# Performance work log

Measured on AMD Instinct MI355X. Metric: run time of the kernel, lower is better.

## Reference

```python
import jax, jax.numpy as jnp
import numpy as np

B, T, C = 2, 2048, 2048
N_HEAD, KV_HEADS = 16, 4
HEAD_DIM = C // N_HEAD  # 128
EPS = 1e-6


def setup_inputs() -> dict:
    key = jax.random.key(0)
    ks = jax.random.split(key, 3)
    x = jax.random.normal(ks[0], (B, T, C), dtype=jnp.float32)
    qkv_out = (N_HEAD + 2 * KV_HEADS) * HEAD_DIM  # 3072
    w_qkv = jax.random.normal(ks[1], (qkv_out, C), dtype=jnp.float32) * 0.02
    w_proj = jax.random.normal(ks[2], (C, C), dtype=jnp.float32) * 0.02
    q_norm_w = jnp.ones((HEAD_DIM,), dtype=jnp.float32)
    k_norm_w = jnp.ones((HEAD_DIM,), dtype=jnp.float32)
    # RoPE frequencies: theta = 10000^{-2i/d}, angles = pos * theta
    inv_freq = 1.0 / (10000.0 ** (np.arange(0, HEAD_DIM, 2, dtype=np.float32) / HEAD_DIM))
    angles = np.arange(T, dtype=np.float32)[:, None] * inv_freq[None, :]  # [T, 64]
    freqs_cos = jnp.asarray(np.cos(angles), dtype=jnp.float32)
    freqs_sin = jnp.asarray(np.sin(angles), dtype=jnp.float32)
    return {"x": x, "w_qkv": w_qkv, "w_proj": w_proj,
            "q_norm_w": q_norm_w, "k_norm_w": k_norm_w,
            "freqs_cos": freqs_cos, "freqs_sin": freqs_sin}


def _rope(t, cos, sin):
    # t: [B, H, T, D]; interpret last dim as D/2 complex pairs (a, b)
    a = t[..., 0::2]
    b = t[..., 1::2]
    oa = a * cos - b * sin
    ob = a * sin + b * cos
    return jnp.stack([oa, ob], axis=-1).reshape(t.shape)


def _rmsnorm(t, w, eps=EPS):
    rms = jnp.sqrt(jnp.mean(t * t, axis=-1, keepdims=True) + eps)
    return w * (t / rms)


def reference(x, w_qkv, w_proj, q_norm_w, k_norm_w, freqs_cos, freqs_sin):
    b, t, c = x.shape
    hd = HEAD_DIM
    qkv = x @ w_qkv.T  # [B, T, 3072]
    q_size = N_HEAD * hd
    kv_size = KV_HEADS * hd
    q = qkv[..., :q_size].reshape(b, t, N_HEAD, hd).transpose(0, 2, 1, 3)
    k = qkv[..., q_size:q_size + kv_size].reshape(b, t, KV_HEADS, hd).transpose(0, 2, 1, 3)
    v = qkv[..., q_size + kv_size:].reshape(b, t, KV_HEADS, hd).transpose(0, 2, 1, 3)
    # repeat_interleave KV heads to match query heads (GQA)
    rep = N_HEAD // KV_HEADS
    k = jnp.repeat(k, rep, axis=1)
    v = jnp.repeat(v, rep, axis=1)
    # RoPE (applied after repeat, matching the torch code order)
    cos = freqs_cos[:t][None, None, :, :]
    sin = freqs_sin[:t][None, None, :, :]
    q = _rope(q, cos, sin)
    k = _rope(k, cos, sin)
    # QK RMSNorm per head_dim
    q = _rmsnorm(q, q_norm_w)
    k = _rmsnorm(k, k_norm_w)
    # causal SDPA
    scores = jnp.einsum('bhqd,bhkd->bhqk', q, k) / jnp.sqrt(jnp.float32(hd))
    causal = jnp.tril(jnp.ones((t, t), dtype=bool))
    scores = jnp.where(causal[None, None], scores, jnp.finfo(scores.dtype).min)
    att = jax.nn.softmax(scores, axis=-1)
    y = jnp.einsum('bhqk,bhkd->bhqd', att, v)
    y = y.transpose(0, 2, 1, 3).reshape(b, t, c)
    return y @ w_proj.T
```

## Files before the change

### kernel.cpp

```cpp
#include <hip/hip_runtime.h>
#include <hip/hip_bf16.h>

#define B_    2
#define T_    2048
#define C_    2048
#define NH_   16
#define KVH_  4
#define HD_   128
#define QKV_  3072
#define M_    4096

typedef float  floatx4 __attribute__((ext_vector_type(4)));
typedef __bf16 bf16x8  __attribute__((ext_vector_type(8)));
typedef __bf16 bf16x4  __attribute__((ext_vector_type(4)));
typedef __bf16 bf16x2  __attribute__((ext_vector_type(2)));

typedef const __attribute__((address_space(1))) void* gas_t;
typedef __attribute__((address_space(3))) void*       las_t;
__device__ __forceinline__ void gl_lds16(const void* g, void* l) {
  __builtin_amdgcn_global_load_lds((gas_t)g, (las_t)l, 16, 0, 0);
}

__global__ __launch_bounds__(256) void cvt3(const float* __restrict__ s0, __bf16* __restrict__ d0, int n0,
                                            const float* __restrict__ s1, __bf16* __restrict__ d1, int n1,
                                            const float* __restrict__ s2, __bf16* __restrict__ d2, int n2) {
  int i = blockIdx.x * blockDim.x + threadIdx.x;
  const float* s; __bf16* d;
  if (i < n0) { s = s0; d = d0; }
  else {
    i -= n0;
    if (i < n1) { s = s1; d = d1; }
    else { i -= n1; if (i >= n2) return; s = s2; d = d2; }
  }
  float4 f = ((const float4*)s)[i];
  bf16x4 o = { (__bf16)f.x, (__bf16)f.y, (__bf16)f.z, (__bf16)f.w };
  ((bf16x4*)d)[i] = o;
}

template <typename OutT>
__global__ __launch_bounds__(256) void gemm_bt(const __bf16* __restrict__ A,
                                               const __bf16* __restrict__ Bm,
                                               OutT* __restrict__ Cc,
                                               int N, int K) {
  __shared__ __align__(16) __bf16 As[2][128 * 32];
  __shared__ __align__(16) __bf16 Bs[2][128 * 32];
  const int tid  = threadIdx.x;
  const int wid  = tid >> 6, lane = tid & 63, quad = lane >> 4, r16 = lane & 15;
  const int bm   = blockIdx.y * 128, bn = blockIdx.x * 128;
  const int wm   = (wid >> 1) * 64, wn = (wid & 1) * 64;
  const int srow = wid * 16 + (lane >> 2);
  const int scol = (lane & 3) * 8;
  const __bf16* aptr = A  + (size_t)(bm + srow) * K + scol;
  const __bf16* bptr = Bm + (size_t)(bn + srow) * K + scol;
  const size_t rowskip = (size_t)64 * K;

  floatx4 acc[4][4];
  #pragma unroll
  for (int i = 0; i < 4; i++)
    #pragma unroll
    for (int j = 0; j < 4; j++) acc[i][j] = (floatx4){0.f, 0.f, 0.f, 0.f};

  for (int k0 = 0; k0 < K; k0 += 64) {
    #pragma unroll
    for (int hf = 0; hf < 2; hf++) {
      gl_lds16(aptr + k0 + hf * 32,           &As[hf][wid * 512]);
      gl_lds16(aptr + rowskip + k0 + hf * 32, &As[hf][2048 + wid * 512]);
      gl_lds16(bptr + k0 + hf * 32,           &Bs[hf][wid * 512]);
      gl_lds16(bptr + rowskip + k0 + hf * 32, &Bs[hf][2048 + wid * 512]);
    }
    __syncthreads();

    #pragma unroll
    for (int hf = 0; hf < 2; hf++) {
      bf16x8 af[4], bfr[4];
      #pragma unroll
      for (int i = 0; i < 4; i++) af[i]  = *(const bf16x8*)&As[hf][(wm + i * 16 + r16) * 32 + quad * 8];
      #pragma unroll
      for (int j = 0; j < 4; j++) bfr[j] = *(const bf16x8*)&Bs[hf][(wn + j * 16 + r16) * 32 + quad * 8];
      #pragma unroll
      for (int i = 0; i < 4; i++)
        #pragma unroll
        for (int j = 0; j < 4; j++)
          acc[i][j] = __builtin_amdgcn_mfma_f32_16x16x32_bf16(af[i], bfr[j], acc[i][j], 0, 0, 0);
    }
    __syncthreads();
  }

  #pragma unroll
  for (int i = 0; i < 4; i++) {
    #pragma unroll
    for (int reg = 0; reg < 4; reg++) {
      int row = bm + wm + i * 16 + quad * 4 + reg;
      OutT* crow = Cc + (size_t)row * N + bn + wn;
      #pragma unroll
      for (int j = 0; j < 4; j++) crow[j * 16 + r16] = (OutT)acc[i][j][reg];
    }
  }
}

__global__ __launch_bounds__(256) void rope_norm(const __bf16* __restrict__ qkv,
                                                 const float* __restrict__ qw,
                                                 const float* __restrict__ kw,
                                                 const float* __restrict__ fc,
                                                 const float* __restrict__ fs,
                                                 __bf16* __restrict__ qn,
                                                 __bf16* __restrict__ kn) {
  const int tid  = threadIdx.x;
  const int wid  = tid >> 6, lane = tid & 63;
  const int row  = blockIdx.x * 4 + wid;
  const int b    = row >> 11, t = row & (T_ - 1);
  const float cs = fc[t * 64 + lane], sn = fs[t * 64 + lane];
  const __bf16* base = qkv + (size_t)row * QKV_;

  #pragma unroll 2
  for (int h = 0; h < NH_; h++) {
    bf16x2 ab = *(const bf16x2*)(base + h * HD_ + 2 * lane);
    float ax = (float)ab[0], ay = (float)ab[1];
    float oa = ax * cs - ay * sn;
    float ob = ax * sn + ay * cs;
    float ss = oa * oa + ob * ob;
    #pragma unroll
    for (int off = 32; off; off >>= 1) ss += __shfl_xor(ss, off);
    float rinv = rsqrtf(ss * (1.0f / HD_) + 1e-6f);
    bf16x2 o = { (__bf16)(oa * rinv * qw[2 * lane]), (__bf16)(ob * rinv * qw[2 * lane + 1]) };
    *(bf16x2*)&qn[(size_t)((b * NH_ + h) * T_ + t) * HD_ + 2 * lane] = o;
  }
  #pragma unroll 2
  for (int h = 0; h < KVH_; h++) {
    bf16x2 ab = *(const bf16x2*)(base + C_ + h * HD_ + 2 * lane);
    float ax = (float)ab[0], ay = (float)ab[1];
    float oa = ax * cs - ay * sn;
    float ob = ax * sn + ay * cs;
    float ss = oa * oa + ob * ob;
    #pragma unroll
    for (int off = 32; off; off >>= 1) ss += __shfl_xor(ss, off);
    float rinv = rsqrtf(ss * (1.0f / HD_) + 1e-6f);
    bf16x2 o = { (__bf16)(oa * rinv * kw[2 * lane]), (__bf16)(ob * rinv * kw[2 * lane + 1]) };
    *(bf16x2*)&kn[(size_t)((b * KVH_ + h) * T_ + t) * HD_ + 2 * lane] = o;
  }
}

__global__ __launch_bounds__(256) void vtrans(const __bf16* __restrict__ qkv,
                                              __bf16* __restrict__ vT) {
  __shared__ __bf16 L[64 * 68];
  const int tid = threadIdx.x;
  const int t0 = blockIdx.x * 64;
  const int d0 = blockIdx.y * 64;
  const int z  = blockIdx.z;
  const int b  = z >> 2, hk = z & 3;
  const int srcc = C_ + KVH_ * HD_ + hk * HD_ + d0;
  const int rr = tid >> 4, c4 = (tid & 15) * 4;
  #pragma unroll
  for (int i = 0; i < 4; i++) {
    int t = rr + i * 16;
    bf16x4 f = *(const bf16x4*)&qkv[(size_t)(b * T_ + t0 + t) * QKV_ + srcc + c4];
    *(bf16x4*)&L[t * 68 + c4] = f;
  }
  __syncthreads();
  const int dr = tid >> 3, tc8 = (tid & 7) * 8;
  #pragma unroll
  for (int i = 0; i < 2; i++) {
    int d = dr + i * 32;
    bf16x8 ov;
    #pragma unroll
    for (int j = 0; j < 8; j++) ov[j] = L[(tc8 + j) * 68 + d];
    *(bf16x8*)&vT[(size_t)(z * HD_ + d0 + d) * T_ + t0 + tc8] = ov;
  }
}

__device__ __forceinline__ int swz_w(int lane) {
  return ((lane & 3) << 4) | ((lane >> 2) ^ ((lane & 3) << 1));
}
__device__ __forceinline__ int swz_r(int quad, int r16) {
  return (quad << 4) | (r16 ^ (quad << 1));
}

__device__ __forceinline__ void kv_prefetch8(const __bf16* kbase, const __bf16* vbase,
                                             int kt0, int wid, int lane,
                                             bf16x8 kreg[2], bf16x8 vreg[2]) {
  const int r4 = lane >> 2, c8 = (lane & 3) * 8;
  #pragma unroll
  for (int i = 0; i < 2; i++) {
    const int n = wid * 2 + i;
    kreg[i] = *(const bf16x8*)&kbase[(size_t)(kt0 + (n >> 2) * 16 + r4) * HD_ + (n & 3) * 32 + c8];
    vreg[i] = *(const bf16x8*)&vbase[(size_t)((n >> 1) * 16 + r4) * T_ + kt0 + (n & 1) * 32 + c8];
  }
}

__device__ __forceinline__ void kv_commit8(__bf16* Ks, __bf16* Vs, int wid, int lane,
                                           const bf16x8 kreg[2], const bf16x8 vreg[2]) {
  const int slot = swz_w(lane);
  #pragma unroll
  for (int i = 0; i < 2; i++) {
    *(bf16x8*)(Ks + (wid * 2 + i) * 512 + slot * 8) = kreg[i];
    *(bf16x8*)(Vs + (wid * 2 + i) * 512 + slot * 8) = vreg[i];
  }
}

__global__ __launch_bounds__(512, 4) void flash(const __bf16* __restrict__ q,
                                                const __bf16* __restrict__ k,
                                                const __bf16* __restrict__ vT,
                                                __bf16* __restrict__ y) {
  __shared__ __align__(16) __bf16 Ks[2][64 * 128];
  __shared__ __align__(16) __bf16 Vs[2][64 * 128];
  __shared__ __align__(16) __bf16 Ps[8][16 * 48];
  const int tid = threadIdx.x;
  const int wid = tid >> 6, lane = tid & 63, quad = lane >> 4, r16 = lane & 15;
  const int x   = blockIdx.x;
  const int p   = (x >> 5) & 7, hl = x & 31;
  const int qt  = (x < 256) ? (15 - p) : p;
  const int b = hl >> 4, h = hl & 15, hk = h >> 2;

  const __bf16* kbase = k  + (size_t)(b * KVH_ + hk) * T_ * HD_;
  const __bf16* vbase = vT + (size_t)(b * KVH_ + hk) * HD_ * T_;
  __bf16* Pw = Ps[wid];
  const float sc = 0.08838834764831845f;
  const float NEG = -__builtin_inff();
  bf16x8 ones;
  #pragma unroll
  for (int i = 0; i < 8; i++) ones[i] = (__bf16)1.0f;

  const int nt = 2 * (qt + 1);
  const int r0 = qt * 128 + wid * 16;

  const __bf16* qrow = q + ((size_t)(b * NH_ + h) * T_ + r0 + r16) * HD_;
  bf16x8 qf[4];
  #pragma unroll
  for (int kb = 0; kb < 4; kb++) qf[kb] = *(const bf16x8*)&qrow[kb * 32 + quad * 8];

  floatx4 o[8], ol = (floatx4){0.f, 0.f, 0.f, 0.f};
  #pragma unroll
  for (int j = 0; j < 8; j++) o[j] = (floatx4){0.f, 0.f, 0.f, 0.f};
  float m_r[4] = {NEG, NEG, NEG, NEG};

  bf16x8 kreg[2], vreg[2];
  kv_prefetch8(kbase, vbase, 0, wid, lane, kreg, vreg);
  kv_commit8(&Ks[0][0], &Vs[0][0], wid, lane, kreg, vreg);
  if (nt > 1) kv_prefetch8(kbase, vbase, 64, wid, lane, kreg, vreg);
  __syncthreads();

  #pragma unroll 1
  for (int it = 0; it < nt; ++it) {
    if (it + 1 < nt) {
      kv_commit8(&Ks[(it + 1) & 1][0], &Vs[(it + 1) & 1][0], wid, lane, kreg, vreg);
      if (it + 2 < nt) kv_prefetch8(kbase, vbase, (it + 2) * 64, wid, lane, kreg, vreg);
    }

    const int kt0 = it * 64;
    const __bf16* Kb = &Ks[it & 1][0];
    const __bf16* Vb = &Vs[it & 1][0];
    if (kt0 <= r0 + 15) {
      floatx4 s[4];
      #pragma unroll
      for (int cb = 0; cb < 4; cb++) s[cb] = (floatx4){0.f, 0.f, 0.f, 0.f};
      __builtin_amdgcn_s_setprio(1);
      #pragma unroll
      for (int kb = 0; kb < 4; kb++)
        #pragma unroll
        for (int cb = 0; cb < 4; cb++) {
          bf16x8 kf = *(const bf16x8*)&Kb[(cb * 4 + kb) * 512 + swz_r(quad, r16) * 8];
          s[cb] = __builtin_amdgcn_mfma_f32_16x16x32_bf16(qf[kb], kf, s[cb], 0, 0, 0);
        }
      __builtin_amdgcn_s_setprio(0);

      const bool needmask = (kt0 + 63 > r0);
      #pragma unroll
      for (int reg = 0; reg < 4; reg++) {
        const int rowq = r0 + quad * 4 + reg;
        s[0][reg] *= sc; s[1][reg] *= sc; s[2][reg] *= sc; s[3][reg] *= sc;
        if (needmask) {
          if (kt0 +      r16 > rowq) s[0][reg] = NEG;
          if (kt0 + 16 + r16 > rowq) s[1][reg] = NEG;
          if (kt0 + 32 + r16 > rowq) s[2][reg] = NEG;
          if (kt0 + 48 + r16 > rowq) s[3][reg] = NEG;
        }
      }
      float mx[4], mnew[4];
      #pragma unroll
      for (int reg = 0; reg < 4; reg++) {
        float m0 = fmaxf(fmaxf(s[0][reg], s[1][reg]), fmaxf(s[2][reg], s[3][reg]));
        #pragma unroll
        for (int off = 8; off; off >>= 1) m0 = fmaxf(m0, __shfl_xor(m0, off));
        mx[reg] = m0;
        mnew[reg] = fmaxf(m_r[reg], m0);
      }
      float growth = fmaxf(fmaxf(mx[0] - m_r[0], mx[1] - m_r[1]),
                           fmaxf(mx[2] - m_r[2], mx[3] - m_r[3]));
      if (!__all(growth <= 8.0f)) {
        #pragma unroll
        for (int reg = 0; reg < 4; reg++) {
          float a = __expf(m_r[reg] - mnew[reg]);
          m_r[reg] = mnew[reg];
          ol[reg] *= a;
          #pragma unroll
          for (int j = 0; j < 8; j++) o[j][reg] *= a;
        }
      }
      #pragma unroll
      for (int c = 0; c < 2; c++) {
        #pragma unroll
        for (int reg = 0; reg < 4; reg++) {
          const int prow = quad * 4 + reg;
          Pw[prow * 48 +      r16] = (__bf16)__expf(s[2 * c    ][reg] - m_r[reg]);
          Pw[prow * 48 + 16 + r16] = (__bf16)__expf(s[2 * c + 1][reg] - m_r[reg]);
        }
        __asm__ volatile("" ::: "memory");
        bf16x8 pf = *(const bf16x8*)&Pw[r16 * 48 + quad * 8];
        __builtin_amdgcn_s_setprio(1);
        ol = __builtin_amdgcn_mfma_f32_16x16x32_bf16(pf, ones, ol, 0, 0, 0);
        #pragma unroll
        for (int j = 0; j < 8; j++) {
          bf16x8 vf = *(const bf16x8*)&Vb[(j * 2 + c) * 512 + swz_r(quad, r16) * 8];
          o[j] = __builtin_amdgcn_mfma_f32_16x16x32_bf16(pf, vf, o[j], 0, 0, 0);
        }
        __builtin_amdgcn_s_setprio(0);
        __asm__ volatile("" ::: "memory");
      }
    }
    __syncthreads();
  }

  #pragma unroll
  for (int reg = 0; reg < 4; reg++) {
    int trow = r0 + quad * 4 + reg;
    float inv = 1.0f / ol[reg];
    __bf16* yr = y + ((size_t)(b * T_) + trow) * C_ + h * HD_;
    #pragma unroll
    for (int j = 0; j < 8; j++) yr[j * 16 + r16] = (__bf16)(o[j][reg] * inv);
  }
}

extern "C" void kernel_launch(void* const* d_in, const int* in_sizes, int n_in,
                              void* d_out, int out_size, void* d_ws, size_t ws_size,
                              hipStream_t stream) {
  const float* x     = (const float*)d_in[0];
  const float* wqkv  = (const float*)d_in[1];
  const float* wproj = (const float*)d_in[2];
  const float* qw    = (const float*)d_in[3];
  const float* kw    = (const float*)d_in[4];
  const float* fc    = (const float*)d_in[5];
  const float* fs    = (const float*)d_in[6];
  float* out = (float*)d_out;

  char* w = (char*)d_ws;
  __bf16* xb     = (__bf16*)w; w += (size_t)M_ * C_ * 2;
  __bf16* wqkvb  = (__bf16*)w; w += (size_t)QKV_ * C_ * 2;
  __bf16* wprojb = (__bf16*)w; w += (size_t)C_ * C_ * 2;
  __bf16* qkv    = (__bf16*)w; w += (size_t)M_ * QKV_ * 2;
  __bf16* qn     = (__bf16*)w; w += (size_t)B_ * NH_ * T_ * HD_ * 2;
  __bf16* kn     = (__bf16*)w; w += (size_t)B_ * KVH_ * T_ * HD_ * 2;
  __bf16* vT     = (__bf16*)w; w += (size_t)B_ * KVH_ * T_ * HD_ * 2;
  __bf16* ybf    = (__bf16*)w; w += (size_t)M_ * C_ * 2;

  const int n0 = M_ * C_ / 4, n1 = QKV_ * C_ / 4, n2 = C_ * C_ / 4;
  cvt3<<<(n0 + n1 + n2 + 255) / 256, 256, 0, stream>>>(x, xb, n0, wqkv, wqkvb, n1, wproj, wprojb, n2);

  gemm_bt<__bf16><<<dim3(QKV_ / 128, M_ / 128), 256, 0, stream>>>(xb, wqkvb, qkv, QKV_, C_);
  rope_norm<<<M_ / 4, 256, 0, stream>>>(qkv, qw, kw, fc, fs, qn, kn);
  vtrans<<<dim3(T_ / 64, HD_ / 64, B_ * KVH_), 256, 0, stream>>>(qkv, vT);
  flash<<<dim3(512), 512, 0, stream>>>(qn, kn, vT, ybf);
  gemm_bt<float><<<dim3(C_ / 128, M_ / 128), 256, 0, stream>>>(ybf, wprojb, out, C_, C_);
}
```

Measured before the change: 322.5 us.

## Add 256x256 tiled GEMM with 10-slot LDS ring pipeline for QKV projection

Adds a new 512-thread GEMM kernel that uses 256x256 output tiles and a 10-slot LDS ring buffer. Half-tiles are staged with direct global-to-LDS loads, interleaved with four MFMA phases per K step, and s_setprio raises priority around the MFMA work. The kernel replaces the 128x128 GEMM for the QKV projection only. Larger tiles improve data reuse, but the grid shrinks to 12x16=192 blocks, fewer than the CU count, so the GPU may be underutilized, and the large shared-memory ring limits occupancy.

```diff
diff --git a/kernel.cpp b/kernel.cpp
--- a/kernel.cpp
+++ b/kernel.cpp
@@ -98,6 +98,165 @@
   }
 }
 
+template <typename OutT>
+__global__ __launch_bounds__(512, 2) void gemm256(const __bf16* __restrict__ A,
+                                                  const __bf16* __restrict__ Bm,
+                                                  OutT* __restrict__ Cc,
+                                                  int N, int K) {
+  __shared__ __align__(16) __bf16 ring[10 * 8192];
+  const int tid  = threadIdx.x;
+  const int lane = tid & 63, quad = lane >> 4, r16 = lane & 15;
+  const int wid  = tid >> 6;
+  const int wm   = wid >> 2, wn = wid & 3;
+  const int bm   = blockIdx.y * 256, bn = blockIdx.x * 256;
+  const int nt   = K >> 6;
+  const int wbase = tid & ~63;
+  const int lb   = (wn & 1) * 4;
+
+  floatx4 acc[8][4];
+  #pragma unroll
+  for (int i = 0; i < 8; i++)
+    #pragma unroll
+    for (int j = 0; j < 4; j++) acc[i][j] = (floatx4){0.f, 0.f, 0.f, 0.f};
+
+  auto stage = [&](int h, int slot) {
+    const int kt = h >> 2, q = h & 3;
+    const __bf16* gb = (q < 2) ? (A  + (size_t)(bm + (q << 7)) * K)
+                               : (Bm + (size_t)(bn + ((q - 2) << 7)) * K);
+    #pragma unroll
+    for (int is = 0; is < 2; is++) {
+      const int s   = is * 512 + tid;
+      const int lrh = s >> 7, cc = (s >> 4) & 7, sl = s & 15;
+      const int lr  = lrh * 16 + (sl ^ cc);
+      gl_lds16(gb + (size_t)lr * K + (kt << 6) + (cc << 3),
+               &ring[slot * 8192 + (is * 512 + wbase) * 8]);
+    }
+  };
+
+  #pragma unroll 1
+  for (int h = 0; h < 6; ++h)
+    if (h < 4 * nt) stage(h, h);
+
+  #pragma unroll 1
+  for (int j = 0; j < nt; ++j) {
+    if (j + 1 < nt) { asm volatile("s_waitcnt vmcnt(4)" ::: "memory"); }
+    else            { asm volatile("s_waitcnt vmcnt(0)" ::: "memory"); }
+    __builtin_amdgcn_s_barrier();
+    asm volatile("" ::: "memory");
+
+    const int b4 = (4 * j) % 10;
+    const __bf16* Ah = &ring[((b4 + wm) % 10) * 8192];
+    const __bf16* Bh = &ring[((b4 + 2 + (wn >> 1)) % 10) * 8192];
+    const int h0 = 4 * j + 6, hend = 4 * nt;
+
+    bf16x8 af[4][2], bfr[2][2];
+
+    #pragma unroll
+    for (int i = 0; i < 4; i++)
+      #pragma unroll
+      for (int ks = 0; ks < 2; ks++) {
+        const int cc = ks * 4 + quad;
+        af[i][ks] = *(const bf16x8*)&Ah[i * 1024 + cc * 128 + ((r16 ^ cc) << 3)];
+      }
+    #pragma unroll
+    for (int i = 0; i < 2; i++)
+      #pragma unroll
+      for (int ks = 0; ks < 2; ks++) {
+        const int cc = ks * 4 + quad;
+        bfr[i][ks] = *(const bf16x8*)&Bh[(lb + i) * 1024 + cc * 128 + ((r16 ^ cc) << 3)];
+      }
+    if (h0 < hend) stage(h0, (b4 + 6) % 10);
+    __builtin_amdgcn_s_barrier();
+    __builtin_amdgcn_s_setprio(1);
+    #pragma unroll
+    for (int ks = 0; ks < 2; ks++)
+      #pragma unroll
+      for (int i = 0; i < 4; i++)
+        #pragma unroll
+        for (int jj = 0; jj < 2; jj++)
+          acc[i][jj] = __builtin_amdgcn_mfma_f32_16x16x32_bf16(af[i][ks], bfr[jj][ks], acc[i][jj], 0, 0, 0);
+    __builtin_amdgcn_s_setprio(0);
+    __builtin_amdgcn_s_barrier();
+
+    #pragma unroll
+    for (int i = 0; i < 2; i++)
+      #pragma unroll
+      for (int ks = 0; ks < 2; ks++) {
+        const int cc = ks * 4 + quad;
+        bfr[i][ks] = *(const bf16x8*)&Bh[(lb + 2 + i) * 1024 + cc * 128 + ((r16 ^ cc) << 3)];
+      }
+    if (h0 + 1 < hend) stage(h0 + 1, (b4 + 7) % 10);
+    __builtin_amdgcn_s_barrier();
+    __builtin_amdgcn_s_setprio(1);
+    #pragma unroll
+    for (int ks = 0; ks < 2; ks++)
+      #pragma unroll
+      for (int i = 0; i < 4; i++)
+        #pragma unroll
+        for (int jj = 0; jj < 2; jj++)
+          acc[i][2 + jj] = __builtin_amdgcn_mfma_f32_16x16x32_bf16(af[i][ks], bfr[jj][ks], acc[i][2 + jj], 0, 0, 0);
+    __builtin_amdgcn_s_setprio(0);
+    __builtin_amdgcn_s_barrier();
+
+    #pragma unroll
+    for (int i = 0; i < 4; i++)
+      #pragma unroll
+      for (int ks = 0; ks < 2; ks++) {
+        const int cc = ks * 4 + quad;
+        af[i][ks] = *(const bf16x8*)&Ah[(4 + i) * 1024 + cc * 128 + ((r16 ^ cc) << 3)];
+      }
+    #pragma unroll
+    for (int i = 0; i < 2; i++)
+      #pragma unroll
+      for (int ks = 0; ks < 2; ks++) {
+        const int cc = ks * 4 + quad;
+        bfr[i][ks] = *(const bf16x8*)&Bh[(lb + i) * 1024 + cc * 128 + ((r16 ^ cc) << 3)];
+      }
+    if (h0 + 2 < hend) stage(h0 + 2, (b4 + 8) % 10);
+    __builtin_amdgcn_s_barrier();
+    __builtin_amdgcn_s_setprio(1);
+    #pragma unroll
+    for (int ks = 0; ks < 2; ks++)
+      #pragma unroll
+      for (int i = 0; i < 4; i++)
+        #pragma unroll
+        for (int jj = 0; jj < 2; jj++)
+          acc[4 + i][jj] = __builtin_amdgcn_mfma_f32_16x16x32_bf16(af[i][ks], bfr[jj][ks], acc[4 + i][jj], 0, 0, 0);
+    __builtin_amdgcn_s_setprio(0);
+    __builtin_amdgcn_s_barrier();
+
+    #pragma unroll
+    for (int i = 0; i < 2; i++)
+      #pragma unroll
+      for (int ks = 0; ks < 2; ks++) {
+        const int cc = ks * 4 + quad;
+        bfr[i][ks] = *(const bf16x8*)&Bh[(lb + 2 + i) * 1024 + cc * 128 + ((r16 ^ cc) << 3)];
+      }
+    if (h0 + 3 < hend) stage(h0 + 3, (b4 + 9) % 10);
+    __builtin_amdgcn_s_barrier();
+    __builtin_amdgcn_s_setprio(1);
+    #pragma unroll
+    for (int ks = 0; ks < 2; ks++)
+      #pragma unroll
+      for (int i = 0; i < 4; i++)
+        #pragma unroll
+        for (int jj = 0; jj < 2; jj++)
+          acc[4 + i][2 + jj] = __builtin_amdgcn_mfma_f32_16x16x32_bf16(af[i][ks], bfr[jj][ks], acc[4 + i][2 + jj], 0, 0, 0);
+    __builtin_amdgcn_s_setprio(0);
+    __builtin_amdgcn_s_barrier();
+  }
+
+  #pragma unroll
+  for (int mi = 0; mi < 8; mi++)
+    #pragma unroll
+    for (int reg = 0; reg < 4; reg++) {
+      const int row = bm + wm * 128 + mi * 16 + quad * 4 + reg;
+      OutT* crow = Cc + (size_t)row * N + bn + wn * 64;
+      #pragma unroll
+      for (int ni = 0; ni < 4; ni++) crow[ni * 16 + r16] = (OutT)acc[mi][ni][reg];
+    }
+}
+
 __global__ __launch_bounds__(256) void rope_norm(const __bf16* __restrict__ qkv,
                                                  const float* __restrict__ qw,
                                                  const float* __restrict__ kw,
@@ -355,7 +514,7 @@
   const int n0 = M_ * C_ / 4, n1 = QKV_ * C_ / 4, n2 = C_ * C_ / 4;
   cvt3<<<(n0 + n1 + n2 + 255) / 256, 256, 0, stream>>>(x, xb, n0, wqkv, wqkvb, n1, wproj, wprojb, n2);
 
-  gemm_bt<__bf16><<<dim3(QKV_ / 128, M_ / 128), 256, 0, stream>>>(xb, wqkvb, qkv, QKV_, C_);
+  gemm256<__bf16><<<dim3(QKV_ / 256, M_ / 256), 512, 0, stream>>>(xb, wqkvb, qkv, QKV_, C_);
   rope_norm<<<M_ / 4, 256, 0, stream>>>(qkv, qw, kw, fc, fs, qn, kn);
   vtrans<<<dim3(T_ / 64, HD_ / 64, B_ * KVH_), 256, 0, stream>>>(qkv, vT);
   flash<<<dim3(512), 512, 0, stream>>>(qn, kn, vT, ybf);
```

Measured after the change: 322.1 us. About the same (-0.1%).

## Double-buffer GEMM LDS with swizzle and vmcnt pipelining; merge rope and V-transpose

Applied to the files above, without the earlier changes.

Rewrites the bf16 GEMM so the next K-tile's global-to-LDS loads are issued before computing on the current tile. It uses two LDS stages of 128x64, an XOR-swizzled layout to avoid bank conflicts, s_waitcnt vmcnt for partial waits, and setprio around the MFMA blocks. It also fuses the rope/RMSNorm and V-transpose kernels into one launch with a block-index split, removing one launch. LDS use doubles to 64KB per block, which may limit occupancy despite launch_bounds(256,2).

```diff
diff --git a/kernel.cpp b/kernel.cpp
--- a/kernel.cpp
+++ b/kernel.cpp
@@ -38,21 +38,21 @@
 }
 
 template <typename OutT>
-__global__ __launch_bounds__(256) void gemm_bt(const __bf16* __restrict__ A,
-                                               const __bf16* __restrict__ Bm,
-                                               OutT* __restrict__ Cc,
-                                               int N, int K) {
-  __shared__ __align__(16) __bf16 As[2][128 * 32];
-  __shared__ __align__(16) __bf16 Bs[2][128 * 32];
+__global__ __launch_bounds__(256, 2) void gemm_cnt(const __bf16* __restrict__ A,
+                                                   const __bf16* __restrict__ Bm,
+                                                   OutT* __restrict__ Cc,
+                                                   int N, int K) {
+  __shared__ __align__(16) __bf16 As[2][128 * 64];
+  __shared__ __align__(16) __bf16 Bs[2][128 * 64];
   const int tid  = threadIdx.x;
   const int wid  = tid >> 6, lane = tid & 63, quad = lane >> 4, r16 = lane & 15;
   const int bm   = blockIdx.y * 128, bn = blockIdx.x * 128;
   const int wm   = (wid >> 1) * 64, wn = (wid & 1) * 64;
-  const int srow = wid * 16 + (lane >> 2);
-  const int scol = (lane & 3) * 8;
-  const __bf16* aptr = A  + (size_t)(bm + srow) * K + scol;
-  const __bf16* bptr = Bm + (size_t)(bn + srow) * K + scol;
-  const size_t rowskip = (size_t)64 * K;
+  const int srow = tid >> 3;
+  const int clog = (tid & 7) ^ (srow & 7);
+  const __bf16* aR = A  + (size_t)(bm + srow) * K + clog * 8;
+  const __bf16* bR = Bm + (size_t)(bn + srow) * K + clog * 8;
+  const int nt = K >> 6;
 
   floatx4 acc[4][4];
   #pragma unroll
@@ -60,30 +60,48 @@
     #pragma unroll
     for (int j = 0; j < 4; j++) acc[i][j] = (floatx4){0.f, 0.f, 0.f, 0.f};
 
-  for (int k0 = 0; k0 < K; k0 += 64) {
+  auto stage = [&](int s, int k0) {
+    #pragma unroll
+    for (int p = 0; p < 4; p++) {
+      gl_lds16(aR + (size_t)(p * 32) * K + k0, &As[s][(p * 32 + wid * 8) * 64]);
+      gl_lds16(bR + (size_t)(p * 32) * K + k0, &Bs[s][(p * 32 + wid * 8) * 64]);
+    }
+  };
+
+  stage(0, 0);
+
+  #pragma unroll 1
+  for (int j = 0; j < nt; ++j) {
+    if (j + 1 < nt) {
+      stage((j + 1) & 1, (j + 1) << 6);
+      asm volatile("s_waitcnt vmcnt(8)" ::: "memory");
+    } else {
+      asm volatile("s_waitcnt vmcnt(0)" ::: "memory");
+    }
+    __builtin_amdgcn_s_barrier();
+    asm volatile("" ::: "memory");
+
+    const __bf16* Ab = As[j & 1];
+    const __bf16* Bb = Bs[j & 1];
     #pragma unroll
     for (int hf = 0; hf < 2; hf++) {
-      gl_lds16(aptr + k0 + hf * 32,           &As[hf][wid * 512]);
-      gl_lds16(aptr + rowskip + k0 + hf * 32, &As[hf][2048 + wid * 512]);
-      gl_lds16(bptr + k0 + hf * 32,           &Bs[hf][wid * 512]);
-      gl_lds16(bptr + rowskip + k0 + hf * 32, &Bs[hf][2048 + wid * 512]);
-    }
-    __syncthreads();
-
-    #pragma unroll
-    for (int hf = 0; hf < 2; hf++) {
+      const int xo = (((hf << 2) + quad) ^ (r16 & 7)) << 3;
       bf16x8 af[4], bfr[4];
       #pragma unroll
-      for (int i = 0; i < 4; i++) af[i]  = *(const bf16x8*)&As[hf][(wm + i * 16 + r16) * 32 + quad * 8];
-      #pragma unroll
-      for (int j = 0; j < 4; j++) bfr[j] = *(const bf16x8*)&Bs[hf][(wn + j * 16 + r16) * 32 + quad * 8];
+      for (int i = 0; i < 4; i++) af[i]  = *(const bf16x8*)&Ab[(wm + i * 16 + r16) * 64 + xo];
+      #pragma unroll
+      for (int i = 0; i < 4; i++) bfr[i] = *(const bf16x8*)&Bb[(wn + i * 16 + r16) * 64 + xo];
+      __builtin_amdgcn_s_setprio(1);
       #pragma unroll
       for (int i = 0; i < 4; i++)
         #pragma unroll
-        for (int j = 0; j < 4; j++)
-          acc[i][j] = __builtin_amdgcn_mfma_f32_16x16x32_bf16(af[i], bfr[j], acc[i][j], 0, 0, 0);
-    }
-    __syncthreads();
+        for (int jj = 0; jj < 4; jj++)
+          acc[i][jj] = __builtin_amdgcn_mfma_f32_16x16x32_bf16(af[i], bfr[jj], acc[i][jj], 0, 0, 0);
+      __builtin_amdgcn_s_setprio(0);
+    }
+    asm volatile("" ::: "memory");
+    __builtin_amdgcn_s_barrier();
+    asm volatile("" ::: "memory");
   }
 
   #pragma unroll
@@ -98,55 +116,55 @@
   }
 }
 
-__global__ __launch_bounds__(256) void rope_norm(const __bf16* __restrict__ qkv,
-                                                 const float* __restrict__ qw,
-                                                 const float* __restrict__ kw,
-                                                 const float* __restrict__ fc,
-                                                 const float* __restrict__ fs,
-                                                 __bf16* __restrict__ qn,
-                                                 __bf16* __restrict__ kn) {
-  const int tid  = threadIdx.x;
-  const int wid  = tid >> 6, lane = tid & 63;
-  const int row  = blockIdx.x * 4 + wid;
-  const int b    = row >> 11, t = row & (T_ - 1);
-  const float cs = fc[t * 64 + lane], sn = fs[t * 64 + lane];
-  const __bf16* base = qkv + (size_t)row * QKV_;
-
-  #pragma unroll 2
-  for (int h = 0; h < NH_; h++) {
-    bf16x2 ab = *(const bf16x2*)(base + h * HD_ + 2 * lane);
-    float ax = (float)ab[0], ay = (float)ab[1];
-    float oa = ax * cs - ay * sn;
-    float ob = ax * sn + ay * cs;
-    float ss = oa * oa + ob * ob;
-    #pragma unroll
-    for (int off = 32; off; off >>= 1) ss += __shfl_xor(ss, off);
-    float rinv = rsqrtf(ss * (1.0f / HD_) + 1e-6f);
-    bf16x2 o = { (__bf16)(oa * rinv * qw[2 * lane]), (__bf16)(ob * rinv * qw[2 * lane + 1]) };
-    *(bf16x2*)&qn[(size_t)((b * NH_ + h) * T_ + t) * HD_ + 2 * lane] = o;
-  }
-  #pragma unroll 2
-  for (int h = 0; h < KVH_; h++) {
-    bf16x2 ab = *(const bf16x2*)(base + C_ + h * HD_ + 2 * lane);
-    float ax = (float)ab[0], ay = (float)ab[1];
-    float oa = ax * cs - ay * sn;
-    float ob = ax * sn + ay * cs;
-    float ss = oa * oa + ob * ob;
-    #pragma unroll
-    for (int off = 32; off; off >>= 1) ss += __shfl_xor(ss, off);
-    float rinv = rsqrtf(ss * (1.0f / HD_) + 1e-6f);
-    bf16x2 o = { (__bf16)(oa * rinv * kw[2 * lane]), (__bf16)(ob * rinv * kw[2 * lane + 1]) };
-    *(bf16x2*)&kn[(size_t)((b * KVH_ + h) * T_ + t) * HD_ + 2 * lane] = o;
-  }
-}
-
-__global__ __launch_bounds__(256) void vtrans(const __bf16* __restrict__ qkv,
+__global__ __launch_bounds__(256) void ropevt(const __bf16* __restrict__ qkv,
+                                              const float* __restrict__ qw,
+                                              const float* __restrict__ kw,
+                                              const float* __restrict__ fc,
+                                              const float* __restrict__ fs,
+                                              __bf16* __restrict__ qn,
+                                              __bf16* __restrict__ kn,
                                               __bf16* __restrict__ vT) {
   __shared__ __bf16 L[64 * 68];
   const int tid = threadIdx.x;
-  const int t0 = blockIdx.x * 64;
-  const int d0 = blockIdx.y * 64;
-  const int z  = blockIdx.z;
+  if (blockIdx.x < M_ / 4) {
+    const int wid  = tid >> 6, lane = tid & 63;
+    const int row  = blockIdx.x * 4 + wid;
+    const int b    = row >> 11, t = row & (T_ - 1);
+    const float cs = fc[t * 64 + lane], sn = fs[t * 64 + lane];
+    const __bf16* base = qkv + (size_t)row * QKV_;
+
+    #pragma unroll 2
+    for (int h = 0; h < NH_; h++) {
+      bf16x2 ab = *(const bf16x2*)(base + h * HD_ + 2 * lane);
+      float ax = (float)ab[0], ay = (float)ab[1];
+      float oa = ax * cs - ay * sn;
+      float ob = ax * sn + ay * cs;
+      float ss = oa * oa + ob * ob;
+      #pragma unroll
+      for (int off = 32; off; off >>= 1) ss += __shfl_xor(ss, off);
+      float rinv = rsqrtf(ss * (1.0f / HD_) + 1e-6f);
+      bf16x2 o = { (__bf16)(oa * rinv * qw[2 * lane]), (__bf16)(ob * rinv * qw[2 * lane + 1]) };
+      *(bf16x2*)&qn[(size_t)((b * NH_ + h) * T_ + t) * HD_ + 2 * lane] = o;
+    }
+    #pragma unroll 2
+    for (int h = 0; h < KVH_; h++) {
+      bf16x2 ab = *(const bf16x2*)(base + C_ + h * HD_ + 2 * lane);
+      float ax = (float)ab[0], ay = (float)ab[1];
+      float oa = ax * cs - ay * sn;
+      float ob = ax * sn + ay * cs;
+      float ss = oa * oa + ob * ob;
+      #pragma unroll
+      for (int off = 32; off; off >>= 1) ss += __shfl_xor(ss, off);
+      float rinv = rsqrtf(ss * (1.0f / HD_) + 1e-6f);
+      bf16x2 o = { (__bf16)(oa * rinv * kw[2 * lane]), (__bf16)(ob * rinv * kw[2 * lane + 1]) };
+      *(bf16x2*)&kn[(size_t)((b * KVH_ + h) * T_ + t) * HD_ + 2 * lane] = o;
+    }
+    return;
+  }
+  const int idx = blockIdx.x - M_ / 4;
+  const int t0 = (idx & 31) * 64;
+  const int d0 = ((idx >> 5) & 1) * 64;
+  const int z  = idx >> 6;
   const int b  = z >> 2, hk = z & 3;
   const int srcc = C_ + KVH_ * HD_ + hk * HD_ + d0;
   const int rr = tid >> 4, c4 = (tid & 15) * 4;
@@ -355,9 +373,8 @@
   const int n0 = M_ * C_ / 4, n1 = QKV_ * C_ / 4, n2 = C_ * C_ / 4;
   cvt3<<<(n0 + n1 + n2 + 255) / 256, 256, 0, stream>>>(x, xb, n0, wqkv, wqkvb, n1, wproj, wprojb, n2);
 
-  gemm_bt<__bf16><<<dim3(QKV_ / 128, M_ / 128), 256, 0, stream>>>(xb, wqkvb, qkv, QKV_, C_);
-  rope_norm<<<M_ / 4, 256, 0, stream>>>(qkv, qw, kw, fc, fs, qn, kn);
-  vtrans<<<dim3(T_ / 64, HD_ / 64, B_ * KVH_), 256, 0, stream>>>(qkv, vT);
+  gemm_cnt<__bf16><<<dim3(QKV_ / 128, M_ / 128), 256, 0, stream>>>(xb, wqkvb, qkv, QKV_, C_);
+  ropevt<<<M_ / 4 + (T_ / 64) * (HD_ / 64) * (B_ * KVH_), 256, 0, stream>>>(qkv, qw, kw, fc, fs, qn, kn, vT);
   flash<<<dim3(512), 512, 0, stream>>>(qn, kn, vT, ybf);
-  gemm_bt<float><<<dim3(C_ / 128, M_ / 128), 256, 0, stream>>>(ybf, wprojb, out, C_, C_);
-}
+  gemm_cnt<float><<<dim3(C_ / 128, M_ / 128), 256, 0, stream>>>(ybf, wprojb, out, C_, C_);
+}
```

Measured after the change: 316.0 us. -2.0%, faster.
